# Performance work log

Measured on AMD Instinct MI355X. Metric: run time of the kernel, lower is better.

## Reference

```python
import jax, jax.numpy as jnp
import numpy as np

DT = 0.5
T_STEPS = int(2500 / DT)   # 5000
T_STIM = int(2000 / DT)    # 4000
A = 270.0; B_ = 108.0; D_ = 0.154; GAMMA = 0.641; TAU_S = 100.0; TAU_AMPA = 2.0
BATCH = 4096


def setup_inputs() -> dict:
    key = jax.random.key(0)
    k0, k1, k2, k3, k4 = jax.random.split(key, 5)
    return {
        "input_signal": jax.random.normal(k0, (BATCH, 1), dtype=jnp.float32),
        "J11": jnp.float32(0.2609), "J12": jnp.float32(0.0497),
        "J21": jnp.float32(0.0497), "J22": jnp.float32(0.2609),
        "J_ext": jnp.float32(0.0156), "I_0": jnp.float32(0.3255),
        "noise_ampa": jnp.float32(0.02), "threshold": jnp.float32(0.5),
        "motor_delay": jnp.float32(0.1),
        "eps0_1": jax.random.normal(k1, (BATCH, 1), dtype=jnp.float32),
        "eps0_2": jax.random.normal(k2, (BATCH, 1), dtype=jnp.float32),
        "eps_1": jax.random.normal(k3, (T_STEPS, BATCH, 1), dtype=jnp.float32),
        "eps_2": jax.random.normal(k4, (T_STEPS, BATCH, 1), dtype=jnp.float32),
    }


def _H(x):
    # Wong-Wang f-I curve: relu((a x - b) / (1 - exp(-d (a x - b)) + 1e-6))
    u = A * x - B_
    return jax.nn.relu(u / (1.0 - jnp.exp(-D_ * u) + 1e-6))


def _simulate(input_signal, J11, J12, J21, J22, J_ext, I_0, noise_ampa,
              eps0_1, eps0_2, eps_1, eps_2):
    decay = jnp.exp(jnp.float32(-DT / TAU_AMPA))
    nscale = jnp.float32(np.sqrt((1.0 - np.exp(-2.0 * DT / TAU_AMPA)) / 2.0))
    s0 = jnp.full_like(input_signal, 0.1)  # [B,1]
    carry0 = (s0, s0, eps0_1 * noise_ampa, eps0_2 * noise_ampa)

    def step(carry, xs):
        s1, s2, In1, In2 = carry
        e1, e2, t = xs
        stim = t < T_STIM
        I1 = jnp.where(stim, J_ext * (1.0 + input_signal / 100.0), 0.0)
        I2 = jnp.where(stim, J_ext * (1.0 - input_signal / 100.0), 0.0)
        x1 = J11 * s1 - J12 * s2 + I_0 + I1 + In1
        x2 = J22 * s2 - J21 * s1 + I_0 + I2 + In2
        ds1 = -(s1 / TAU_S) + (1.0 - s1) * _H(x1) * GAMMA / 1000.0
        ds2 = -(s2 / TAU_S) + (1.0 - s2) * _H(x2) * GAMMA / 1000.0
        In1n = In1 * decay + noise_ampa * nscale * e1
        In2n = In2 * decay + noise_ampa * nscale * e2
        s1n = s1 + ds1 * DT
        s2n = s2 + ds2 * DT
        ys = (jnp.concatenate([s1n, s2n], axis=-1),   # trajectory row [B,2]
              jnp.concatenate([ds1, ds2], axis=-1))   # dsdt row [B,2]
        return (s1n, s2n, In1n, In2n), ys

    ts = jnp.arange(T_STEPS)
    _, (traj, dsdt) = jax.lax.scan(step, carry0, (eps_1, eps_2, ts))
    return traj, dsdt  # each [T, B, 2]


def _decide(traj_m):
    # traj_m = trajectory - threshold; first-crossing times per unit
    m1 = traj_m[:, :, 0] > 0
    m2 = traj_m[:, :, 1] > 0
    inf = jnp.float32(jnp.inf)
    t1 = jnp.where(m1.any(0), jnp.argmax(m1, axis=0).astype(jnp.float32), inf)
    t2 = jnp.where(m2.any(0), jnp.argmax(m2, axis=0).astype(jnp.float32), inf)
    dtimes = jnp.where(t1 < t2, t1, -t2)
    return dtimes * DT


def reference(input_signal, J11, J12, J21, J22, J_ext, I_0, noise_ampa,
              threshold, motor_delay, eps0_1, eps0_2, eps_1, eps_2):
    traj, dsdt = _simulate(input_signal, J11, J12, J21, J22, J_ext, I_0,
                           noise_ampa, eps0_1, eps0_2, eps_1, eps_2)
    out = _decide(traj - threshold)  # [B], signed decision time in ms
    out = jnp.where(out < 0, out / 1000.0 - motor_delay,
                    jnp.where(out > 0, out / 1000.0 + motor_delay, out))
    return out
```

## Files before the change

### kernel.cpp

```cpp
#include <hip/hip_runtime.h>

#define BATCHN 4096
#define NSTEPS 5000
#define NSTIM  4000
#define U      25
#define NBLK      (NSTEPS / U)
#define NBLK_STIM (NSTIM / U)

__global__ __launch_bounds__(128, 1) void ww_kernel(
    const float* __restrict__ input_signal,
    const float* __restrict__ sJ11, const float* __restrict__ sJ12,
    const float* __restrict__ sJ21, const float* __restrict__ sJ22,
    const float* __restrict__ sJext, const float* __restrict__ sI0,
    const float* __restrict__ sNoise, const float* __restrict__ sThr,
    const float* __restrict__ sDelay,
    const float* __restrict__ eps0_1, const float* __restrict__ eps0_2,
    const float* __restrict__ eps_1, const float* __restrict__ eps_2,
    float* __restrict__ out)
{
    __shared__ float4 slab[2][U][64];
    __shared__ int flag;

    const int tid  = threadIdx.x;
    const int lane = tid & 63;
    const int b    = blockIdx.x * 64 + lane;

    const float noise = sNoise[0];
    const float Jext = sJext[0], I0 = sI0[0];
    const float KE = -0.22217503629690245f;

    const float inp = input_signal[b];
    const float P1s = fmaf(270.0f, I0 + Jext * (1.0f + inp * 0.01f), -108.0f);
    const float P2s = fmaf(270.0f, I0 + Jext * (1.0f - inp * 0.01f), -108.0f);
    const float Pn  = fmaf(270.0f, I0, -108.0f);

    if (tid >= 64) {
        const float decay = 0.7788007830714049f;
        const float kN270 = noise * 0.4435478165294536f * 270.0f;
        const float* __restrict__ p1 = eps_1 + b;
        const float* __restrict__ p2 = eps_2 + b;
        float V1 = eps0_1[b] * noise * 270.0f;
        float V2 = eps0_2[b] * noise * 270.0f;

        auto fill = [&](int blk) {
            const int sl = blk & 1;
            const size_t off = (size_t)blk * U * BATCHN;
            const bool stim = (blk < NBLK_STIM);
            const float P1 = stim ? P1s : Pn;
            const float P2 = stim ? P2s : Pn;
            float r1[U], r2[U];
            #pragma unroll
            for (int i = 0; i < U; ++i) {
                r1[i] = p1[off + (size_t)i * BATCHN];
                r2[i] = p2[off + (size_t)i * BATCHN];
            }
            #pragma unroll
            for (int i = 0; i < U; ++i) {
                float C1 = V1 + P1;
                float C2 = V2 + P2;
                slab[sl][i][lane] = make_float4(C1, C2, KE * C1, KE * C2);
                V1 = fmaf(V1, decay, kN270 * r1[i]);
                V2 = fmaf(V2, decay, kN270 * r2[i]);
            }
        };

        fill(0);
        __syncthreads();
        for (int blk = 0; blk < NBLK; ++blk) {
            if (blk + 1 < NBLK) fill(blk + 1);
            __syncthreads();
            if (flag) break;
        }
        return;
    }

    __builtin_amdgcn_s_setprio(3);
    const float J11 = sJ11[0], J12 = sJ12[0], J21 = sJ21[0], J22 = sJ22[0];
    const float thr = sThr[0], delay = sDelay[0];

    const float A11 = 270.0f * J11, nA12 = -270.0f * J12;
    const float A22 = 270.0f * J22, nA21 = -270.0f * J21;
    const float B11 = KE * A11, B12 = KE * nA12;
    const float B22 = KE * A22, B21 = KE * nA21;
    const float SM = 0.995f;
    const float QC = 3.205e-4f;
    const float INF = __builtin_inff();

    float s1 = 0.1f, s2 = 0.1f;
    float tm1 = INF, tm2 = INF;
    float tf = 0.0f;

    if (tid == 0) flag = 0;
    __syncthreads();
    bool done = false;
    for (int blk = 0; blk < NBLK && !done; ++blk) {
        const float4* __restrict__ base = &slab[blk & 1][0][lane];
        float4 d0 = base[0];
        float4 d1 = base[64];
        #pragma unroll
        for (int i = 0; i < U; ++i) {
            float4 cu = d0;
            d0 = d1;
            if (i + 2 < U) d1 = base[(i + 2) * 64];
            float u1 = fmaf(A11, s1, fmaf(nA12, s2, cu.x));
            float u2 = fmaf(A22, s2, fmaf(nA21, s1, cu.y));
            float w1 = fmaf(B11, s1, fmaf(B12, s2, cu.z));
            float w2 = fmaf(B22, s2, fmaf(B21, s1, cu.w));
            float x1 = __builtin_amdgcn_exp2f(w1);
            float x2 = __builtin_amdgcn_exp2f(w2);
            float r1 = __builtin_amdgcn_rcpf(1.000001f - x1);
            float r2 = __builtin_amdgcn_rcpf(1.000001f - x2);
            float h1 = fmaxf(u1 * r1, 0.0f);
            float h2 = fmaxf(u2 * r2, 0.0f);
            s1 = fmaf(h1, fmaf(-QC, s1, QC), SM * s1);
            s2 = fmaf(h2, fmaf(-QC, s2, QC), SM * s2);
            tm1 = fminf(tm1, (s1 > thr) ? tf : INF);
            tm2 = fminf(tm2, (s2 > thr) ? tf : INF);
            tf += 1.0f;
        }
        done = __all((tm1 < INF) || (tm2 < INF));
        if (done && lane == 0) flag = 1;
        __syncthreads();
    }

    float o;
    if (tm1 == INF && tm2 == INF) {
        o = -3.0e38f;
    } else {
        float dtm = (tm1 < tm2) ? tm1 : -tm2;
        o = dtm * 0.5f;
        if (o < 0.0f)      o = o / 1000.0f - delay;
        else if (o > 0.0f) o = o / 1000.0f + delay;
    }
    out[b] = o;
}

extern "C" void kernel_launch(void* const* d_in, const int* in_sizes, int n_in,
                              void* d_out, int out_size, void* d_ws, size_t ws_size,
                              hipStream_t stream) {
    ww_kernel<<<dim3(BATCHN / 64), dim3(128), 0, stream>>>(
        (const float*)d_in[0],
        (const float*)d_in[1],
        (const float*)d_in[2],
        (const float*)d_in[3],
        (const float*)d_in[4],
        (const float*)d_in[5],
        (const float*)d_in[6],
        (const float*)d_in[7],
        (const float*)d_in[8],
        (const float*)d_in[9],
        (const float*)d_in[10],
        (const float*)d_in[11],
        (const float*)d_in[12],
        (const float*)d_in[13],
        (float*)d_out);
}
```

Before: 471.2 us.

## Move threshold scanning to producer warp and shrink per-step LDS input

The compute wavefront no longer checks the threshold or tracks first-crossing times. It writes its state pairs to a double-buffered LDS trajectory buffer, and the producer wavefront scans them one block later, setting the early-exit flag. Producer slabs shrink from float4 to float2, with the KE multiply moved back into the compute step, and become triple-buffered so prefetch can cross block boundaries. This trims the serial critical path and LDS read width, at the cost of an extra multiply per step, more LDS writes, and early exit detected one block later.

```diff
diff --git a/kernel.cpp b/kernel.cpp
--- a/kernel.cpp
+++ b/kernel.cpp
@@ -3,7 +3,7 @@
 #define BATCHN 4096
 #define NSTEPS 5000
 #define NSTIM  4000
-#define U      25
+#define U      20
 #define NBLK      (NSTEPS / U)
 #define NBLK_STIM (NSTIM / U)
 
@@ -18,7 +18,8 @@
     const float* __restrict__ eps_1, const float* __restrict__ eps_2,
     float* __restrict__ out)
 {
-    __shared__ float4 slab[2][U][64];
+    __shared__ float2 slab[3][U][64];
+    __shared__ float4 traj[2][U / 2][64];
     __shared__ int flag;
 
     const int tid  = threadIdx.x;
@@ -28,111 +29,132 @@
     const float noise = sNoise[0];
     const float Jext = sJext[0], I0 = sI0[0];
     const float KE = -0.22217503629690245f;
-
-    const float inp = input_signal[b];
-    const float P1s = fmaf(270.0f, I0 + Jext * (1.0f + inp * 0.01f), -108.0f);
-    const float P2s = fmaf(270.0f, I0 + Jext * (1.0f - inp * 0.01f), -108.0f);
-    const float Pn  = fmaf(270.0f, I0, -108.0f);
+    const float INF = __builtin_inff();
 
     if (tid >= 64) {
         const float decay = 0.7788007830714049f;
         const float kN270 = noise * 0.4435478165294536f * 270.0f;
+        const float thr = sThr[0], delay = sDelay[0];
+        const float inp = input_signal[b];
+        const float P1s = fmaf(270.0f, I0 + Jext * (1.0f + inp * 0.01f), -108.0f);
+        const float P2s = fmaf(270.0f, I0 + Jext * (1.0f - inp * 0.01f), -108.0f);
+        const float Pn  = fmaf(270.0f, I0, -108.0f);
         const float* __restrict__ p1 = eps_1 + b;
         const float* __restrict__ p2 = eps_2 + b;
         float V1 = eps0_1[b] * noise * 270.0f;
         float V2 = eps0_2[b] * noise * 270.0f;
+        float tm1 = INF, tm2 = INF;
 
-        auto fill = [&](int blk) {
-            const int sl = blk & 1;
-            const size_t off = (size_t)blk * U * BATCHN;
-            const bool stim = (blk < NBLK_STIM);
-            const float P1 = stim ? P1s : Pn;
-            const float P2 = stim ? P2s : Pn;
-            float r1[U], r2[U];
+        auto loadblk = [&](int j, float* r1, float* r2) {
+            const size_t off = (size_t)j * U * BATCHN;
             #pragma unroll
             for (int i = 0; i < U; ++i) {
                 r1[i] = p1[off + (size_t)i * BATCHN];
                 r2[i] = p2[off + (size_t)i * BATCHN];
             }
+        };
+        auto storeblk = [&](int j, const float* r1, const float* r2) {
+            const int sl = j % 3;
+            const float P1 = (j < NBLK_STIM) ? P1s : Pn;
+            const float P2 = (j < NBLK_STIM) ? P2s : Pn;
             #pragma unroll
             for (int i = 0; i < U; ++i) {
-                float C1 = V1 + P1;
-                float C2 = V2 + P2;
-                slab[sl][i][lane] = make_float4(C1, C2, KE * C1, KE * C2);
+                slab[sl][i][lane] = make_float2(V1 + P1, V2 + P2);
                 V1 = fmaf(V1, decay, kN270 * r1[i]);
                 V2 = fmaf(V2, decay, kN270 * r2[i]);
             }
         };
+        auto scanblk = [&](int j) {
+            const int par = j & 1;
+            float tf = (float)(j * U);
+            #pragma unroll
+            for (int i2 = 0; i2 < U / 2; ++i2) {
+                float4 v = traj[par][i2][lane];
+                tm1 = fminf(tm1, (v.x > thr) ? tf : INF);
+                tm2 = fminf(tm2, (v.y > thr) ? tf : INF);
+                tm1 = fminf(tm1, (v.z > thr) ? (tf + 1.0f) : INF);
+                tm2 = fminf(tm2, (v.w > thr) ? (tf + 1.0f) : INF);
+                tf += 2.0f;
+            }
+        };
 
-        fill(0);
+        {
+            float r1[U], r2[U];
+            loadblk(0, r1, r2); storeblk(0, r1, r2);
+            loadblk(1, r1, r2); storeblk(1, r1, r2);
+        }
         __syncthreads();
-        for (int blk = 0; blk < NBLK; ++blk) {
-            if (blk + 1 < NBLK) fill(blk + 1);
+        for (int k = 0;; ++k) {
+            float r1[U], r2[U];
+            const bool dofill = (k + 2) < NBLK;
+            if (dofill) loadblk(k + 2, r1, r2);
+            if (k >= 1) {
+                scanblk(k - 1);
+                if (__all((tm1 < INF) || (tm2 < INF)) && lane == 0) flag = 1;
+            }
+            if (dofill) storeblk(k + 2, r1, r2);
             __syncthreads();
-            if (flag) break;
+            if (flag || k + 1 == NBLK) break;
         }
+        if (!flag) scanblk(NBLK - 1);
+
+        float o;
+        if (tm1 == INF && tm2 == INF) {
+            o = -3.0e38f;
+        } else {
+            float dtm = (tm1 < tm2) ? tm1 : -tm2;
+            o = dtm * 0.5f;
+            if (o < 0.0f)      o = o / 1000.0f - delay;
+            else if (o > 0.0f) o = o / 1000.0f + delay;
+        }
+        out[b] = o;
         return;
     }
 
     __builtin_amdgcn_s_setprio(3);
     const float J11 = sJ11[0], J12 = sJ12[0], J21 = sJ21[0], J22 = sJ22[0];
-    const float thr = sThr[0], delay = sDelay[0];
-
     const float A11 = 270.0f * J11, nA12 = -270.0f * J12;
     const float A22 = 270.0f * J22, nA21 = -270.0f * J21;
-    const float B11 = KE * A11, B12 = KE * nA12;
-    const float B22 = KE * A22, B21 = KE * nA21;
     const float SM = 0.995f;
     const float QC = 3.205e-4f;
-    const float INF = __builtin_inff();
 
     float s1 = 0.1f, s2 = 0.1f;
-    float tm1 = INF, tm2 = INF;
-    float tf = 0.0f;
+
+    auto step = [&](float2 c) {
+        float u1 = fmaf(A11, s1, fmaf(nA12, s2, c.x));
+        float u2 = fmaf(A22, s2, fmaf(nA21, s1, c.y));
+        float x1 = __builtin_amdgcn_exp2f(KE * u1);
+        float x2 = __builtin_amdgcn_exp2f(KE * u2);
+        float r1 = __builtin_amdgcn_rcpf(1.000001f - x1);
+        float r2 = __builtin_amdgcn_rcpf(1.000001f - x2);
+        float h1 = fmaxf(u1 * r1, 0.0f);
+        float h2 = fmaxf(u2 * r2, 0.0f);
+        s1 = fmaf(fmaf(-QC, s1, QC), h1, SM * s1);
+        s2 = fmaf(fmaf(-QC, s2, QC), h2, SM * s2);
+    };
 
     if (tid == 0) flag = 0;
     __syncthreads();
-    bool done = false;
-    for (int blk = 0; blk < NBLK && !done; ++blk) {
-        const float4* __restrict__ base = &slab[blk & 1][0][lane];
-        float4 d0 = base[0];
-        float4 d1 = base[64];
+    const float2* __restrict__ lanebase = &slab[0][0][lane];
+    float2 d0 = lanebase[0];
+    float2 d1 = lanebase[64];
+    for (int k = 0;; ++k) {
+        const float2* __restrict__ cb = lanebase + (size_t)(k % 3) * U * 64;
+        const float2* __restrict__ nb = lanebase + (size_t)((k + 1) % 3) * U * 64;
+        float4* __restrict__ tb = &traj[k & 1][0][lane];
         #pragma unroll
-        for (int i = 0; i < U; ++i) {
-            float4 cu = d0;
-            d0 = d1;
-            if (i + 2 < U) d1 = base[(i + 2) * 64];
-            float u1 = fmaf(A11, s1, fmaf(nA12, s2, cu.x));
-            float u2 = fmaf(A22, s2, fmaf(nA21, s1, cu.y));
-            float w1 = fmaf(B11, s1, fmaf(B12, s2, cu.z));
-            float w2 = fmaf(B22, s2, fmaf(B21, s1, cu.w));
-            float x1 = __builtin_amdgcn_exp2f(w1);
-            float x2 = __builtin_amdgcn_exp2f(w2);
-            float r1 = __builtin_amdgcn_rcpf(1.000001f - x1);
-            float r2 = __builtin_amdgcn_rcpf(1.000001f - x2);
-            float h1 = fmaxf(u1 * r1, 0.0f);
-            float h2 = fmaxf(u2 * r2, 0.0f);
-            s1 = fmaf(h1, fmaf(-QC, s1, QC), SM * s1);
-            s2 = fmaf(h2, fmaf(-QC, s2, QC), SM * s2);
-            tm1 = fminf(tm1, (s1 > thr) ? tf : INF);
-            tm2 = fminf(tm2, (s2 > thr) ? tf : INF);
-            tf += 1.0f;
+        for (int i = 0; i < U; i += 2) {
+            float2 n0 = (i + 2 < U) ? cb[(i + 2) * 64] : nb[0];
+            step(d0);
+            float sa1 = s1, sa2 = s2;
+            float2 n1 = (i + 3 < U) ? cb[(i + 3) * 64] : nb[64];
+            step(d1);
+            tb[(i >> 1) * 64] = make_float4(sa1, sa2, s1, s2);
+            d0 = n0; d1 = n1;
         }
-        done = __all((tm1 < INF) || (tm2 < INF));
-        if (done && lane == 0) flag = 1;
         __syncthreads();
+        if (flag || k + 1 == NBLK) break;
     }
-
-    float o;
-    if (tm1 == INF && tm2 == INF) {
-        o = -3.0e38f;
-    } else {
-        float dtm = (tm1 < tm2) ? tm1 : -tm2;
-        o = dtm * 0.5f;
-        if (o < 0.0f)      o = o / 1000.0f - delay;
-        else if (o > 0.0f) o = o / 1000.0f + delay;
-    }
-    out[b] = o;
 }
 
 extern "C" void kernel_launch(void* const* d_in, const int* in_sizes, int n_in,
```

Result: slower. 486.7 us (+3.3%).
